# Performance work log

Measured on AMD Instinct MI355X. Metric: run time of the kernel, lower is better.

## Reference

```python
import jax, jax.numpy as jnp
import numpy as np

B, N, D, H, FF = 40, 257, 1024, 16, 4096
HD = D // H
SCALE = HD ** -0.5


def _layernorm(x, w, b, eps=1e-5):
    mu = jnp.mean(x, axis=-1, keepdims=True)
    var = jnp.var(x, axis=-1, keepdims=True)
    return (x - mu) * jax.lax.rsqrt(var + eps) * w + b


def _quick_gelu(x):
    return x * jax.nn.sigmoid(1.702 * x)


def setup_inputs() -> dict:
    key = jax.random.key(0)
    ks = jax.random.split(key, 8)
    s = 0.02
    return {
        'hidden_states': jax.random.normal(ks[0], (B, N, D), jnp.float32),
        'ln1_w': jnp.ones((D,), jnp.float32),
        'ln1_b': jnp.zeros((D,), jnp.float32),
        'wq': jax.random.normal(ks[1], (D, D), jnp.float32) * s,
        'bq': jnp.zeros((D,), jnp.float32),
        'wk': jax.random.normal(ks[2], (D, D), jnp.float32) * s,
        'bk': jnp.zeros((D,), jnp.float32),
        'wv': jax.random.normal(ks[3], (D, D), jnp.float32) * s,
        'bv': jnp.zeros((D,), jnp.float32),
        'wo': jax.random.normal(ks[4], (D, D), jnp.float32) * s,
        'bo': jnp.zeros((D,), jnp.float32),
        'ln2_w': jnp.ones((D,), jnp.float32),
        'ln2_b': jnp.zeros((D,), jnp.float32),
        'fc1_w': jax.random.normal(ks[5], (FF, D), jnp.float32) * s,
        'fc1_b': jnp.zeros((FF,), jnp.float32),
        'fc2_w': jax.random.normal(ks[6], (D, FF), jnp.float32) * s,
        'fc2_b': jnp.zeros((D,), jnp.float32),
    }


def reference(hidden_states, ln1_w, ln1_b, wq, bq, wk, bk, wv, bv, wo, bo,
              ln2_w, ln2_b, fc1_w, fc1_b, fc2_w, fc2_b):
    bsz, n, dim = hidden_states.shape
    residual = hidden_states
    x = _layernorm(hidden_states, ln1_w, ln1_b)
    # QKV projections (torch Linear: y = x @ W^T + b)
    q = (x @ wq.T + bq) * SCALE
    k = x @ wk.T + bk
    v = x @ wv.T + bv
    # [b, h, n, hd]
    q = q.reshape(bsz, n, H, HD).transpose(0, 2, 1, 3)
    k = k.reshape(bsz, n, H, HD).transpose(0, 2, 1, 3)
    v = v.reshape(bsz, n, H, HD).transpose(0, 2, 1, 3)
    scores = jnp.einsum('bhqd,bhkd->bhqk', q, k)  # [b,h,n,n]
    attn = jax.nn.softmax(scores, axis=-1)
    out = jnp.einsum('bhqk,bhkd->bhqd', attn, v)
    out = out.transpose(0, 2, 1, 3).reshape(bsz, n, dim)
    out = out @ wo.T + bo
    hidden = residual + out
    residual = hidden
    h2 = _layernorm(hidden, ln2_w, ln2_b)
    h2 = _quick_gelu(h2 @ fc1_w.T + fc1_b)
    h2 = h2 @ fc2_w.T + fc2_b
    return residual + h2
```

## Files before the change

kernel.cpp:

```cpp
#include <hip/hip_runtime.h>
#include <math.h>

#define D_DIM 1024
#define FF_DIM 4096
#define N_SEQ 257
#define B_SZ 40
#define H_CNT 16
#define HD_DIM 64
#define M_TOK (B_SZ * N_SEQ)
#define VT_NP 320

typedef unsigned short u16;
typedef unsigned char u8;
typedef __bf16 bf16x8 __attribute__((ext_vector_type(8)));
typedef float f32x4 __attribute__((ext_vector_type(4)));
typedef int i32x4 __attribute__((ext_vector_type(4)));

__device__ __forceinline__ float b2f(u16 u) {
    union { unsigned int i; float f; } x; x.i = ((unsigned int)u) << 16; return x.f;
}
__device__ __forceinline__ u16 f2b(float f) {
    union { float f; unsigned int i; } x; x.f = f;
    unsigned int r = x.i + 0x7FFFu + ((x.i >> 16) & 1u);
    return (u16)(r >> 16);
}
__device__ __forceinline__ unsigned q8(float f, float s) {
    int q = __float2int_rn(f * s);
    q = q < -127 ? -127 : (q > 127 ? 127 : q);
    return (unsigned)q & 0xFFu;
}

__device__ __forceinline__ void g2lds16(const void* g, void* l) {
    __builtin_amdgcn_global_load_lds(
        (const __attribute__((address_space(1))) void*)g,
        (__attribute__((address_space(3))) void*)l,
        16, 0, 0);
}

__global__ __launch_bounds__(256)
void cvt_all_kernel(const float* __restrict__ wq, const float* __restrict__ wk,
                    const float* __restrict__ wv, const float* __restrict__ wo,
                    const float* __restrict__ w1, const float* __restrict__ w2,
                    const float* __restrict__ bq, const float* __restrict__ bk,
                    const float* __restrict__ bv,
                    u16* __restrict__ wdst, u8* __restrict__ w1i8,
                    u8* __restrict__ w2i8, float* __restrict__ bqkv) {
    const int nDD = D_DIM * D_DIM, nFD = FF_DIM * D_DIM;
    const int WB8 = (4 * nDD) / 8;
    const int WF8 = (2 * nFD) / 8;
    const int tid = blockIdx.x * 256 + threadIdx.x;
    if (tid < WB8) {
        const int i = tid * 8;
        const float* src; int s;
        if (i < nDD)          { src = wq; s = i; }
        else if (i < 2 * nDD) { src = wk; s = i - nDD; }
        else if (i < 3 * nDD) { src = wv; s = i - 2 * nDD; }
        else                  { src = wo; s = i - 3 * nDD; }
        float4 a = *(const float4*)(src + s);
        float4 b = *(const float4*)(src + s + 4);
        u16 o[8] = {f2b(a.x), f2b(a.y), f2b(a.z), f2b(a.w),
                    f2b(b.x), f2b(b.y), f2b(b.z), f2b(b.w)};
        *(uint4*)(wdst + i) = *(const uint4*)o;
    } else if (tid < WB8 + WF8) {
        const int j = (tid - WB8) * 8;
        const float* src; u8* dst; int s;
        if (j < nFD) { src = w1; dst = w1i8; s = j; }
        else         { src = w2; dst = w2i8; s = j - nFD; }
        float4 a = *(const float4*)(src + s);
        float4 b = *(const float4*)(src + s + 4);
        const float sc = 1024.f;
        unsigned lo = q8(a.x, sc) | (q8(a.y, sc) << 8) |
                      (q8(a.z, sc) << 16) | (q8(a.w, sc) << 24);
        unsigned hi = q8(b.x, sc) | (q8(b.y, sc) << 8) |
                      (q8(b.z, sc) << 16) | (q8(b.w, sc) << 24);
        uint2 pk = {lo, hi};
        *(uint2*)(dst + s) = pk;
    } else {
        const int j = tid - WB8 - WF8;
        if (j < 3 * D_DIM) {
            bqkv[j] = (j < D_DIM) ? bq[j]
                    : (j < 2 * D_DIM ? bk[j - D_DIM] : bv[j - 2 * D_DIM]);
        }
    }
}

template <bool I8OUT>
__global__ __launch_bounds__(256)
void ln_kernel(const float* __restrict__ in, const float* __restrict__ w,
               const float* __restrict__ b, void* __restrict__ out) {
    const int row = blockIdx.x;
    const int t = threadIdx.x;
    const size_t base = (size_t)row * D_DIM;
    float x[4];
#pragma unroll
    for (int i = 0; i < 4; ++i) x[i] = in[base + t + i * 256];
    float s  = x[0] + x[1] + x[2] + x[3];
    float ss = x[0]*x[0] + x[1]*x[1] + x[2]*x[2] + x[3]*x[3];
#pragma unroll
    for (int o = 32; o > 0; o >>= 1) {
        s  += __shfl_xor(s, o, 64);
        ss += __shfl_xor(ss, o, 64);
    }
    __shared__ float sh_s[4], sh_ss[4];
    const int wave = t >> 6, lane = t & 63;
    if (lane == 0) { sh_s[wave] = s; sh_ss[wave] = ss; }
    __syncthreads();
    float S  = sh_s[0] + sh_s[1] + sh_s[2] + sh_s[3];
    float SS = sh_ss[0] + sh_ss[1] + sh_ss[2] + sh_ss[3];
    float mean = S * (1.0f / D_DIM);
    float var  = SS * (1.0f / D_DIM) - mean * mean;
    float rstd = rsqrtf(var + 1e-5f);
#pragma unroll
    for (int i = 0; i < 4; ++i) {
        int idx = t + i * 256;
        float y = (x[i] - mean) * rstd * w[idx] + b[idx];
        if (I8OUT) ((u8*)out)[base + idx]  = (u8)q8(y, 16.f);
        else       ((u16*)out)[base + idx] = f2b(y);
    }
}

#define G256_PHASE(BUF, KH, KT_S, KH_S, DOSTAGE)                                     \
  {                                                                                  \
    const u16* sa_ = lds + ((BUF) * 4 + (KH)) * 8192;                                \
    const u16* sb_ = lds + ((BUF) * 4 + 2 + (KH)) * 8192;                            \
    bf16x8 af[4], bfv[4];                                                            \
    _Pragma("unroll") for (int mf = 0; mf < 4; ++mf)                                 \
        af[mf] = *(const bf16x8*)(sa_ + (wr * 128 + mf * 16 + l16) * 32 + xch);      \
    _Pragma("unroll") for (int nf = 0; nf < 4; ++nf)                                 \
        bfv[nf] = *(const bf16x8*)(sb_ + (wc * 64 + nf * 16 + l16) * 32 + xch);      \
    if (DOSTAGE) { stageA(KT_S, KH_S); stageB(KT_S, KH_S); }                         \
    __builtin_amdgcn_s_setprio(1);                                                   \
    _Pragma("unroll") for (int mf = 0; mf < 4; ++mf)                                 \
      _Pragma("unroll") for (int nf = 0; nf < 4; ++nf)                               \
          acc[mf][nf] = __builtin_amdgcn_mfma_f32_16x16x32_bf16(                     \
              af[mf], bfv[nf], acc[mf][nf], 0, 0, 0);                                \
    _Pragma("unroll") for (int mf = 0; mf < 4; ++mf)                                 \
        af[mf] = *(const bf16x8*)(sa_ + (wr * 128 + 64 + mf * 16 + l16) * 32 + xch); \
    _Pragma("unroll") for (int mf = 0; mf < 4; ++mf)                                 \
      _Pragma("unroll") for (int nf = 0; nf < 4; ++nf)                               \
          acc[4 + mf][nf] = __builtin_amdgcn_mfma_f32_16x16x32_bf16(                 \
              af[mf], bfv[nf], acc[4 + mf][nf], 0, 0, 0);                            \
    __builtin_amdgcn_s_setprio(0);                                                   \
    asm volatile("s_waitcnt vmcnt(8)" ::: "memory");                                 \
    __builtin_amdgcn_s_barrier();                                                    \
    asm volatile("" ::: "memory");                                                   \
  }

template <int MODE>
__global__ __launch_bounds__(512, 2)
void gemm256_kernel(const u16* __restrict__ A, const u16* __restrict__ Bt,
                    const float* __restrict__ bias, const float* __restrict__ extra,
                    void* __restrict__ out, u16* __restrict__ out2, u16* __restrict__ out3,
                    int M, int N, int K) {
    __shared__ __align__(16) u16 lds[8 * 8192];
    const int t = threadIdx.x;
    const int lane = t & 63, wave = t >> 6;
    const int quad = lane >> 4, l16 = lane & 15;
    const int wr = wave >> 2, wc = wave & 3;
    const int xch = (quad ^ ((l16 >> 1) & 3)) * 8;

    const int nwg = gridDim.x;
    const int nT = N >> 8;
    const int orig = blockIdx.x;
    const int xcd = orig & 7, loc = orig >> 3;
    const int qq = nwg >> 3, rr = nwg & 7;
    const int wgid = (xcd < rr ? xcd * (qq + 1) : rr * (qq + 1) + (xcd - rr) * qq) + loc;
    const int m0 = (wgid / nT) * 256;
    const int n0 = (wgid % nT) * 256;

    auto stageA = [&](int kt, int kh) {
#pragma unroll
        for (int l = 0; l < 2; ++l) {
            const int c = l * 512 + t;
            int gr = m0 + (c >> 2); if (gr > M - 1) gr = M - 1;
            const int sg = (c & 3) ^ ((c >> 3) & 3);
            g2lds16(A + (size_t)gr * K + kt * 64 + kh * 32 + sg * 8,
                    lds + ((kt & 1) * 4 + kh) * 8192 + c * 8);
        }
    };
    auto stageB = [&](int kt, int kh) {
#pragma unroll
        for (int l = 0; l < 2; ++l) {
            const int c = l * 512 + t;
            const int sg = (c & 3) ^ ((c >> 3) & 3);
            g2lds16(Bt + (size_t)(n0 + (c >> 2)) * K + kt * 64 + kh * 32 + sg * 8,
                    lds + ((kt & 1) * 4 + 2 + kh) * 8192 + c * 8);
        }
    };

    f32x4 acc[8][4];
#pragma unroll
    for (int mi = 0; mi < 8; ++mi)
#pragma unroll
        for (int nf = 0; nf < 4; ++nf) acc[mi][nf] = {0.f, 0.f, 0.f, 0.f};

    stageA(0, 0); stageB(0, 0); stageA(0, 1); stageB(0, 1); stageA(1, 0); stageB(1, 0);
    asm volatile("s_waitcnt vmcnt(8)" ::: "memory");
    __builtin_amdgcn_s_barrier();
    asm volatile("" ::: "memory");

    const int NIT = K >> 7;
    for (int i = 0; i < NIT; ++i) {
        const int kt0 = 2 * i;
        const bool more = (i < NIT - 1);
        G256_PHASE(0, 0, kt0 + 1, 1, true)
        G256_PHASE(0, 1, kt0 + 2, 0, more)
        G256_PHASE(1, 0, kt0 + 2, 1, more)
        G256_PHASE(1, 1, kt0 + 3, 0, more)
    }

#pragma unroll
    for (int mi = 0; mi < 8; ++mi) {
#pragma unroll
        for (int nf = 0; nf < 4; ++nf) {
            const int n = n0 + wc * 64 + nf * 16 + l16;
            const float bvf = bias[n];
#pragma unroll
            for (int i2 = 0; i2 < 4; ++i2) {
                const int m = m0 + wr * 128 + mi * 16 + quad * 4 + i2;
                if (m >= M) continue;
                float v = acc[mi][nf][i2] + bvf;
                if (MODE == 2) {
                    const size_t idx = (size_t)m * N + n;
                    ((float*)out)[idx] = extra[idx] + v;
                } else {
                    const int seg = n >> 10, nl = n & 1023;
                    if (seg == 0) {
                        ((u16*)out)[(size_t)m * D_DIM + nl] = f2b(v * 0.125f);
                    } else if (seg == 1) {
                        out2[(size_t)m * D_DIM + nl] = f2b(v);
                    } else {
                        const int bb = m / N_SEQ;
                        const int tt = m - bb * N_SEQ;
                        out3[((size_t)bb * D_DIM + nl) * VT_NP + tt] = f2b(v);
                    }
                }
            }
        }
    }
}

template <int MODE>
__global__ __launch_bounds__(256)
void gemm_i8_kernel(const u8* __restrict__ A, const u8* __restrict__ Bt,
                    const float* __restrict__ bias, const float* __restrict__ extra,
                    void* __restrict__ out, int M, int N, int K, int sw) {
    __shared__ __align__(16) u8 sA[128 * 128];
    __shared__ __align__(16) u8 sB[128 * 128];
    const int t = threadIdx.x;

    const int nM = gridDim.x, nN = gridDim.y;
    const int lid   = blockIdx.y * nM + blockIdx.x;
    const int csz   = sw * nN;
    const int chunk = lid / csz;
    const int rem   = lid - chunk * csz;
    const int n0 = (rem % nN) * 128;
    const int m0 = (chunk * sw + rem / nN) * 128;

    const int wave = t >> 6, lane = t & 63;
    const int quad = lane >> 4, l16 = lane & 15;
    const int wm = (wave >> 1) * 64, wn = (wave & 1) * 64;

    const u8* gA[4]; const u8* gB[4]; u8* lA[4]; u8* lB[4];
#pragma unroll
    for (int i = 0; i < 4; ++i) {
        const int c = i * 256 + t;
        const int row = c >> 3;
        const int sg = (c & 7) ^ (row & 7);
        int gr = m0 + row; if (gr > M - 1) gr = M - 1;
        gA[i] = A  + (size_t)gr * K + sg * 16;
        gB[i] = Bt + (size_t)(n0 + row) * K + sg * 16;
        lA[i] = sA + c * 16;
        lB[i] = sB + c * 16;
    }

    i32x4 acc[4][4];
#pragma unroll
    for (int mt = 0; mt < 4; ++mt)
#pragma unroll
        for (int nt = 0; nt < 4; ++nt) acc[mt][nt] = {0, 0, 0, 0};

    for (int k0 = 0; k0 < K; k0 += 128) {
        __syncthreads();
#pragma unroll
        for (int i = 0; i < 4; ++i) g2lds16(gA[i] + k0, lA[i]);
#pragma unroll
        for (int i = 0; i < 4; ++i) g2lds16(gB[i] + k0, lB[i]);
        __syncthreads();
#pragma unroll
        for (int j = 0; j < 2; ++j) {
            i32x4 af[4], bfr[4];
#pragma unroll
            for (int mt = 0; mt < 4; ++mt) {
                const int r = wm + mt * 16 + l16;
                af[mt] = *(const i32x4*)(sA + r * 128 + (((j * 4 + quad) ^ (r & 7)) * 16));
            }
#pragma unroll
            for (int nt = 0; nt < 4; ++nt) {
                const int n = wn + nt * 16 + l16;
                bfr[nt] = *(const i32x4*)(sB + n * 128 + (((j * 4 + quad) ^ (n & 7)) * 16));
            }
#pragma unroll
            for (int mt = 0; mt < 4; ++mt)
#pragma unroll
                for (int nt = 0; nt < 4; ++nt)
                    acc[mt][nt] = __builtin_amdgcn_mfma_i32_16x16x64_i8(
                        af[mt], bfr[nt], acc[mt][nt], 0, 0, 0);
        }
    }

    const float sc = (MODE == 2) ? (1.f / 32768.f) : (1.f / 16384.f);
#pragma unroll
    for (int mt = 0; mt < 4; ++mt) {
#pragma unroll
        for (int nt = 0; nt < 4; ++nt) {
            const int n = n0 + wn + nt * 16 + l16;
            const float bvf = bias[n];
#pragma unroll
            for (int i = 0; i < 4; ++i) {
                const int m = m0 + wm + quad * 4 + i + mt * 16;
                if (m >= M) continue;
                float v = (float)acc[mt][nt][i] * sc + bvf;
                if (MODE == 2) {
                    const size_t idx = (size_t)m * N + n;
                    ((float*)out)[idx] = extra[idx] + v;
                } else {
                    float g = v / (1.0f + __expf(-1.702f * v));
                    ((u8*)out)[(size_t)m * N + n] = (u8)q8(g, 32.f);
                }
            }
        }
    }
}

#define ATT_PS 296
#define ATT_KROWS 272
__global__ __launch_bounds__(256, 4)
void attn_mfma_kernel(const u16* __restrict__ q, const u16* __restrict__ k,
                      const u16* __restrict__ vT, u16* __restrict__ o) {
    __shared__ __align__(16) u16 sU[64 * ATT_PS];
    __shared__ float sInv[64];
    u16* const sK = sU;
    u16* const sP = sU;

    const int t = threadIdx.x;
    const int wave = t >> 6, lane = t & 63;
    const int quad = lane >> 4, l16 = lane & 15;

    const int lid = blockIdx.x;
    const int g = lid / 40, local = lid - g * 40;
    const int qt = local >> 3, x = local & 7;
    const int hb = g * 8 + x;
    const int h = hb & (H_CNT - 1), b = hb >> 4;
    const int q0 = qt * 64;
    const size_t head = (size_t)b * N_SEQ * D_DIM + (size_t)h * HD_DIM;

    const u16* khead = k + head;
#pragma unroll
    for (int p = 0; p < 9; ++p) {
        const int c = p * 256 + t;
        if (c < ATT_KROWS * 8) {
            const int row = c >> 3;
            const int gr = row > N_SEQ - 1 ? N_SEQ - 1 : row;
            const int sg = (c & 7) ^ (row & 7);
            g2lds16(khead + (size_t)gr * D_DIM + sg * 8, sK + c * 8);
        }
    }

    int qrow = q0 + wave * 16 + l16; if (qrow > N_SEQ - 1) qrow = N_SEQ - 1;
    const u16* qp = q + head + (size_t)qrow * D_DIM + quad * 8;
    bf16x8 qf0 = *(const bf16x8*)(qp);
    bf16x8 qf1 = *(const bf16x8*)(qp + 32);

    asm volatile("s_waitcnt vmcnt(0)" ::: "memory");
    __syncthreads();

    const int xc0 = (quad ^ (l16 & 7)) * 8;
    const int xc1 = ((quad + 4) ^ (l16 & 7)) * 8;
    f32x4 s[5][4];
#pragma unroll
    for (int kt = 0; kt < 5; ++kt) {
        const int ntMax = (kt == 4) ? 2 : 4;
#pragma unroll
        for (int nt = 0; nt < 4; ++nt) {
            if (nt >= ntMax) continue;
            s[kt][nt] = {0.f, 0.f, 0.f, 0.f};
            const int key = kt * 64 + nt * 16 + l16;
            const u16* kr = sK + key * 64;
            bf16x8 b0 = *(const bf16x8*)(kr + xc0);
            bf16x8 b1 = *(const bf16x8*)(kr + xc1);
            s[kt][nt] = __builtin_amdgcn_mfma_f32_16x16x32_bf16(qf0, b0, s[kt][nt], 0, 0, 0);
            s[kt][nt] = __builtin_amdgcn_mfma_f32_16x16x32_bf16(qf1, b1, s[kt][nt], 0, 0, 0);
        }
    }
    __syncthreads();

#pragma unroll
    for (int i = 0; i < 4; ++i) {
        float mx = -1e30f;
#pragma unroll
        for (int kt = 0; kt < 5; ++kt) {
            const int ntMax = (kt == 4) ? 2 : 4;
#pragma unroll
            for (int nt = 0; nt < 4; ++nt) {
                if (nt >= ntMax) continue;
                const bool valid = (kt < 4) || (nt == 0 && l16 == 0);
                if (valid) mx = fmaxf(mx, s[kt][nt][i]);
            }
        }
        mx = fmaxf(mx, __shfl_xor(mx, 1, 64));
        mx = fmaxf(mx, __shfl_xor(mx, 2, 64));
        mx = fmaxf(mx, __shfl_xor(mx, 4, 64));
        mx = fmaxf(mx, __shfl_xor(mx, 8, 64));
        float sum = 0.f;
        const int prow = wave * 16 + quad * 4 + i;
#pragma unroll
        for (int kt = 0; kt < 5; ++kt) {
            const int ntMax = (kt == 4) ? 2 : 4;
#pragma unroll
            for (int nt = 0; nt < 4; ++nt) {
                if (nt >= ntMax) continue;
                const bool valid = (kt < 4) || (nt == 0 && l16 == 0);
                float pv = 0.f;
                if (valid) { pv = __expf(s[kt][nt][i] - mx); sum += pv; }
                sP[prow * ATT_PS + kt * 64 + nt * 16 + l16] = f2b(pv);
            }
        }
        sum += __shfl_xor(sum, 1, 64);
        sum += __shfl_xor(sum, 2, 64);
        sum += __shfl_xor(sum, 4, 64);
        sum += __shfl_xor(sum, 8, 64);
        if (l16 == 0) sInv[prow] = 1.0f / sum;
    }
    __syncthreads();

    f32x4 oacc[4] = {{0.f,0.f,0.f,0.f},{0.f,0.f,0.f,0.f},
                     {0.f,0.f,0.f,0.f},{0.f,0.f,0.f,0.f}};
    const u16* vhead = vT + ((size_t)b * D_DIM + h * HD_DIM) * VT_NP;
    const int prr = wave * 16 + l16;
#pragma unroll
    for (int kt = 0; kt < 5; ++kt) {
        const int j0 = kt * 64;
        bf16x8 p0 = *(const bf16x8*)(sP + prr * ATT_PS + j0 + quad * 8);
        bf16x8 p1;
        if (kt < 4) p1 = *(const bf16x8*)(sP + prr * ATT_PS + j0 + quad * 8 + 32);
#pragma unroll
        for (int nt = 0; nt < 4; ++nt) {
            const u16* vr = vhead + (size_t)(nt * 16 + l16) * VT_NP + j0 + quad * 8;
            bf16x8 b0 = *(const bf16x8*)(vr);
            oacc[nt] = __builtin_amdgcn_mfma_f32_16x16x32_bf16(p0, b0, oacc[nt], 0, 0, 0);
            if (kt < 4) {
                bf16x8 b1 = *(const bf16x8*)(vr + 32);
                oacc[nt] = __builtin_amdgcn_mfma_f32_16x16x32_bf16(p1, b1, oacc[nt], 0, 0, 0);
            }
        }
    }
#pragma unroll
    for (int nt = 0; nt < 4; ++nt) {
#pragma unroll
        for (int i = 0; i < 4; ++i) {
            const int mrow = wave * 16 + quad * 4 + i;
            const int m = q0 + mrow;
            if (m < N_SEQ) {
                o[head + (size_t)m * D_DIM + nt * 16 + l16] =
                    f2b(oacc[nt][i] * sInv[mrow]);
            }
        }
    }
}

extern "C" void kernel_launch(void* const* d_in, const int* in_sizes, int n_in,
                              void* d_out, int out_size, void* d_ws, size_t ws_size,
                              hipStream_t stream) {
    const float* hs   = (const float*)d_in[0];
    const float* ln1w = (const float*)d_in[1];
    const float* ln1b = (const float*)d_in[2];
    const float* wq   = (const float*)d_in[3];
    const float* bq   = (const float*)d_in[4];
    const float* wk   = (const float*)d_in[5];
    const float* bk   = (const float*)d_in[6];
    const float* wv   = (const float*)d_in[7];
    const float* bv   = (const float*)d_in[8];
    const float* wo   = (const float*)d_in[9];
    const float* bo   = (const float*)d_in[10];
    const float* ln2w = (const float*)d_in[11];
    const float* ln2b = (const float*)d_in[12];
    const float* w1   = (const float*)d_in[13];
    const float* b1   = (const float*)d_in[14];
    const float* w2   = (const float*)d_in[15];
    const float* b2   = (const float*)d_in[16];

    char* p = (char*)d_ws;
    size_t off = 0;
    auto alloc = [&](size_t bytes) {
        char* r = p + off;
        off += (bytes + 255) & ~(size_t)255;
        return (void*)r;
    };
    const int M = M_TOK;
    u16* wqkvb = (u16*)alloc((size_t)3 * D_DIM * D_DIM * 2);
    u16* wob   = (u16*)alloc((size_t)D_DIM * D_DIM * 2);
    u8*  w1i8  = (u8*) alloc((size_t)FF_DIM * D_DIM);
    u8*  w2i8  = (u8*) alloc((size_t)D_DIM * FF_DIM);
    float* bqkv = (float*)alloc((size_t)3 * D_DIM * 4);
    u16*  x_ln = (u16*) alloc((size_t)M * D_DIM * 2);
    u16*  qb   = (u16*) alloc((size_t)M * D_DIM * 2);
    u16*  kb   = (u16*) alloc((size_t)M * D_DIM * 2);
    u16*  vTb  = (u16*) alloc((size_t)B_SZ * D_DIM * VT_NP * 2);
    u16*  ab   = (u16*) alloc((size_t)M * D_DIM * 2);
    float* hid = (float*)alloc((size_t)M * D_DIM * 4);
    u8* h1i8 = (u8*)qb;
    u8* x2i8 = (u8*)ab;

    const int nDD = D_DIM * D_DIM, nFD = FF_DIM * D_DIM;
    const int WB8 = (4 * nDD) / 8, WF8 = (2 * nFD) / 8;
    cvt_all_kernel<<<(WB8 + WF8 + 3 * D_DIM + 255) / 256, 256, 0, stream>>>(
        wq, wk, wv, wo, w1, w2, bq, bk, bv, wqkvb, w1i8, w2i8, bqkv);

    ln_kernel<false><<<M, 256, 0, stream>>>(hs, ln1w, ln1b, x_ln);

    const int gM256 = (M + 255) / 256;
    gemm256_kernel<5><<<gM256 * (3 * D_DIM / 256), 512, 0, stream>>>(
        x_ln, wqkvb, bqkv, nullptr, qb, kb, vTb, M, 3 * D_DIM, D_DIM);

    attn_mfma_kernel<<<5 * H_CNT * B_SZ, 256, 0, stream>>>(qb, kb, vTb, ab);

    gemm256_kernel<2><<<gM256 * (D_DIM / 256), 512, 0, stream>>>(
        ab, wob, bo, hs, hid, nullptr, nullptr, M, D_DIM, D_DIM);

    ln_kernel<true><<<M, 256, 0, stream>>>(hid, ln2w, ln2b, x2i8);

    const int gM = (M + 127) / 128;
    dim3 gF(gM, FF_DIM / 128);
    gemm_i8_kernel<3><<<gF, 256, 0, stream>>>(x2i8, w1i8, b1, nullptr, h1i8,
                                              M, FF_DIM, D_DIM, 16);
    dim3 gD(gM, D_DIM / 128);
    gemm_i8_kernel<2><<<gD, 256, 0, stream>>>(h1i8, w2i8, b2, hid, (float*)d_out,
                                              M, D_DIM, FF_DIM, 4);
}
```

Before: 615.0 us.

## Add 256x256-tile int8 MFMA GEMM with pipelined LDS staging for FC1

Replaces the 128x128 int8 GEMM used for the FC1 layer (with fused quick-GELU and int8 requantization) with a new 512-thread kernel using 256x256 output tiles. The new kernel double-buffers K-halves in LDS via direct global-to-LDS loads, overlaps staging with 16x16x64 int8 MFMA bursts under raised wave priority, and remaps workgroups across XCDs. It aims for more data reuse per tile and better overlap of memory and compute. In exchange it needs more LDS and registers per block, and the larger tiles leave a ragged last M tile.

Result: slower. 719.9 us (+17.0%).

```diff
diff --git a/kernel.cpp b/kernel.cpp
--- a/kernel.cpp
+++ b/kernel.cpp
@@ -240,6 +240,113 @@
     }
 }
 
+#define GI8_PHASE(BUF, KH, KT_S, KH_S, DOSTAGE)                                      \
+  {                                                                                  \
+    const u8* sa_ = ldsb + ((BUF) * 4 + (KH)) * 16384;                               \
+    const u8* sb_ = ldsb + ((BUF) * 4 + 2 + (KH)) * 16384;                           \
+    i32x4 af[4], bfv[4];                                                             \
+    _Pragma("unroll") for (int mf = 0; mf < 4; ++mf)                                 \
+        af[mf] = *(const i32x4*)(sa_ + (wr * 128 + mf * 16 + l16) * 64 + xch);       \
+    _Pragma("unroll") for (int nf = 0; nf < 4; ++nf)                                 \
+        bfv[nf] = *(const i32x4*)(sb_ + (wc * 64 + nf * 16 + l16) * 64 + xch);       \
+    if (DOSTAGE) { stageA(KT_S, KH_S); stageB(KT_S, KH_S); }                         \
+    __builtin_amdgcn_s_setprio(1);                                                   \
+    _Pragma("unroll") for (int mf = 0; mf < 4; ++mf)                                 \
+      _Pragma("unroll") for (int nf = 0; nf < 4; ++nf)                               \
+          acc[mf][nf] = __builtin_amdgcn_mfma_i32_16x16x64_i8(                       \
+              af[mf], bfv[nf], acc[mf][nf], 0, 0, 0);                                \
+    _Pragma("unroll") for (int mf = 0; mf < 4; ++mf)                                 \
+        af[mf] = *(const i32x4*)(sa_ + (wr * 128 + 64 + mf * 16 + l16) * 64 + xch);  \
+    _Pragma("unroll") for (int mf = 0; mf < 4; ++mf)                                 \
+      _Pragma("unroll") for (int nf = 0; nf < 4; ++nf)                               \
+          acc[4 + mf][nf] = __builtin_amdgcn_mfma_i32_16x16x64_i8(                   \
+              af[mf], bfv[nf], acc[4 + mf][nf], 0, 0, 0);                            \
+    __builtin_amdgcn_s_setprio(0);                                                   \
+    asm volatile("s_waitcnt vmcnt(8)" ::: "memory");                                 \
+    __builtin_amdgcn_s_barrier();                                                    \
+    asm volatile("" ::: "memory");                                                   \
+  }
+
+__global__ __launch_bounds__(512, 2)
+void gemm_i8_256_kernel(const u8* __restrict__ A, const u8* __restrict__ Bt,
+                        const float* __restrict__ bias, u8* __restrict__ out,
+                        int M, int N, int K) {
+    __shared__ __align__(16) u8 ldsb[8 * 16384];
+    const int t = threadIdx.x;
+    const int lane = t & 63, wave = t >> 6;
+    const int quad = lane >> 4, l16 = lane & 15;
+    const int wr = wave >> 2, wc = wave & 3;
+    const int xch = (quad ^ ((l16 >> 1) & 3)) * 16;
+
+    const int nwg = gridDim.x;
+    const int nT = N >> 8;
+    const int orig = blockIdx.x;
+    const int xcd = orig & 7, loc = orig >> 3;
+    const int qq = nwg >> 3, rr = nwg & 7;
+    const int wgid = (xcd < rr ? xcd * (qq + 1) : rr * (qq + 1) + (xcd - rr) * qq) + loc;
+    const int m0 = (wgid / nT) * 256;
+    const int n0 = (wgid % nT) * 256;
+
+    auto stageA = [&](int kt, int kh) {
+#pragma unroll
+        for (int l = 0; l < 2; ++l) {
+            const int c = l * 512 + t;
+            int gr = m0 + (c >> 2); if (gr > M - 1) gr = M - 1;
+            const int sg = (c & 3) ^ ((c >> 3) & 3);
+            g2lds16(A + (size_t)gr * K + kt * 128 + kh * 64 + sg * 16,
+                    ldsb + ((kt & 1) * 4 + kh) * 16384 + c * 16);
+        }
+    };
+    auto stageB = [&](int kt, int kh) {
+#pragma unroll
+        for (int l = 0; l < 2; ++l) {
+            const int c = l * 512 + t;
+            const int sg = (c & 3) ^ ((c >> 3) & 3);
+            g2lds16(Bt + (size_t)(n0 + (c >> 2)) * K + kt * 128 + kh * 64 + sg * 16,
+                    ldsb + ((kt & 1) * 4 + 2 + kh) * 16384 + c * 16);
+        }
+    };
+
+    i32x4 acc[8][4];
+#pragma unroll
+    for (int mi = 0; mi < 8; ++mi)
+#pragma unroll
+        for (int nf = 0; nf < 4; ++nf) acc[mi][nf] = {0, 0, 0, 0};
+
+    stageA(0, 0); stageB(0, 0); stageA(0, 1); stageB(0, 1); stageA(1, 0); stageB(1, 0);
+    asm volatile("s_waitcnt vmcnt(8)" ::: "memory");
+    __builtin_amdgcn_s_barrier();
+    asm volatile("" ::: "memory");
+
+    const int NIT = K >> 8;
+    for (int i = 0; i < NIT; ++i) {
+        const int kt0 = 2 * i;
+        const bool more = (i < NIT - 1);
+        GI8_PHASE(0, 0, kt0 + 1, 1, true)
+        GI8_PHASE(0, 1, kt0 + 2, 0, more)
+        GI8_PHASE(1, 0, kt0 + 2, 1, more)
+        GI8_PHASE(1, 1, kt0 + 3, 0, more)
+    }
+
+    const float sc = 1.f / 16384.f;
+#pragma unroll
+    for (int mi = 0; mi < 8; ++mi) {
+#pragma unroll
+        for (int nf = 0; nf < 4; ++nf) {
+            const int n = n0 + wc * 64 + nf * 16 + l16;
+            const float bvf = bias[n];
+#pragma unroll
+            for (int i2 = 0; i2 < 4; ++i2) {
+                const int m = m0 + wr * 128 + mi * 16 + quad * 4 + i2;
+                if (m >= M) continue;
+                float v = (float)acc[mi][nf][i2] * sc + bvf;
+                float g = v / (1.0f + __expf(-1.702f * v));
+                out[(size_t)m * N + n] = (u8)q8(g, 32.f);
+            }
+        }
+    }
+}
+
 template <int MODE>
 __global__ __launch_bounds__(256)
 void gemm_i8_kernel(const u8* __restrict__ A, const u8* __restrict__ Bt,
@@ -530,10 +637,10 @@
 
     ln_kernel<true><<<M, 256, 0, stream>>>(hid, ln2w, ln2b, x2i8);
 
+    gemm_i8_256_kernel<<<gM256 * (FF_DIM / 256), 512, 0, stream>>>(
+        x2i8, w1i8, b1, h1i8, M, FF_DIM, D_DIM);
+
     const int gM = (M + 127) / 128;
-    dim3 gF(gM, FF_DIM / 128);
-    gemm_i8_kernel<3><<<gF, 256, 0, stream>>>(x2i8, w1i8, b1, nullptr, h1i8,
-                                              M, FF_DIM, D_DIM, 16);
     dim3 gD(gM, D_DIM / 128);
     gemm_i8_kernel<2><<<gD, 256, 0, stream>>>(h1i8, w2i8, b2, hid, (float*)d_out,
                                               M, D_DIM, FF_DIM, 4);
```
